# Kernel tuning notes

Measured on AMD Instinct MI355X. Metric: run time of the kernel, lower is better.

The kernel has to match this reference:

```python
import jax, jax.numpy as jnp
import numpy as np

N_SRC = 100000
N_DST = 20000
E = 1250000
D_IN = 64
D_OUT = 64
NEG_SLOPE = 0.2  # PyG GATConv default


def setup_inputs() -> dict:
    key = jax.random.key(0)
    ks = jax.random.split(key, 8)
    x = jax.random.normal(ks[0], (N_SRC, D_IN), dtype=jnp.float32)
    res_n_id = jax.random.randint(ks[1], (N_DST,), 0, N_SRC)
    edge_src = jax.random.randint(ks[2], (E,), 0, N_SRC)
    edge_dst = jax.random.randint(ks[3], (E,), 0, N_DST)
    W = jax.random.normal(ks[4], (D_IN, D_OUT), dtype=jnp.float32) / np.sqrt(D_IN)
    att_src = jax.random.normal(ks[5], (D_OUT,), dtype=jnp.float32)
    att_dst = jax.random.normal(ks[6], (D_OUT,), dtype=jnp.float32)
    bias = jax.random.normal(ks[7], (D_OUT,), dtype=jnp.float32) * 0.01
    return {"x": x, "res_n_id": res_n_id, "edge_src": edge_src,
            "edge_dst": edge_dst, "W": W, "att_src": att_src,
            "att_dst": att_dst, "bias": bias}


def reference(x, res_n_id, edge_src, edge_dst, W, att_src, att_dst, bias):
    # Shared linear transform (in_channels is an int -> one weight in PyG)
    h_src = x @ W                      # [N_src, D_OUT]
    h_dst = x[res_n_id] @ W            # [N_dst, D_OUT]
    # Per-node attention logits
    a_src = h_src @ att_src            # [N_src]
    a_dst = h_dst @ att_dst            # [N_dst]
    # Per-edge attention score (gather)
    e = jax.nn.leaky_relu(a_src[edge_src] + a_dst[edge_dst], NEG_SLOPE)  # [E]
    # Segment softmax over incoming edges of each destination node
    m = jax.ops.segment_max(e, edge_dst, num_segments=N_DST)             # [N_dst]
    ex = jnp.exp(e - m[edge_dst])
    denom = jax.ops.segment_sum(ex, edge_dst, num_segments=N_DST)        # [N_dst]
    alpha = ex / (denom[edge_dst] + 1e-16)                               # [E]
    # (dropout on alpha is eval-mode identity)
    # Weighted scatter-aggregate
    msg = h_src[edge_src] * alpha[:, None]                               # [E, D_OUT]
    out = jax.ops.segment_sum(msg, edge_dst, num_segments=N_DST)         # [N_dst, D_OUT]
    return out + bias
```

## Files before the change

kernel.cpp:

```cpp
#include <hip/hip_runtime.h>

#define N_SRC 100000
#define N_DST 20000
#define NE    1250000
#define D     64
#define NEG_SLOPE 0.2f

#define NBKT 2500
#define BCAP 768
#define TILE 4096
#define GEMM_BLKS 391
#define ADST_BLKS 79

__device__ __forceinline__ unsigned short f2bf(float f) {
    unsigned u = __float_as_uint(f);
    u += 0x7FFFu + ((u >> 16) & 1);
    return (unsigned short)(u >> 16);
}
__device__ __forceinline__ float blo(unsigned u) { return __uint_as_float(u << 16); }
__device__ __forceinline__ float bhi(unsigned u) { return __uint_as_float(u & 0xFFFF0000u); }

__global__ __launch_bounds__(256) void k_pre(const float* __restrict__ W,
                                             const float* __restrict__ att_src,
                                             const float* __restrict__ att_dst,
                                             const float* __restrict__ x,
                                             const int* __restrict__ res_n_id,
                                             unsigned short* __restrict__ xb,
                                             float* __restrict__ a_src,
                                             float* __restrict__ a_dst) {
    __shared__ __align__(16) float wL[D];
    int t = threadIdx.x, blk = blockIdx.x;
    bool isA = blk < GEMM_BLKS;
    if (t < D) {
        const float* att = isA ? att_src : att_dst;
        float s = 0.f;
#pragma unroll
        for (int c = 0; c < D; ++c) s += W[t * D + c] * att[c];
        wL[t] = s;
    }
    __syncthreads();
    const float4* x4 = (const float4*)x;
    if (isA) {
        int w = t >> 6, lane = t & 63;
        int row0 = blk * 256 + w * 64;
        ushort4* xb4 = (ushort4*)xb;
        float4 wv = *((const float4*)wL + (lane & 15));
#pragma unroll 4
        for (int it = 0; it < 16; ++it) {
            int r4 = row0 + it * 4;
            if (r4 >= N_SRC) break;
            float4 v = x4[(size_t)r4 * 16 + lane];
            ushort4 o;
            o.x = f2bf(v.x); o.y = f2bf(v.y); o.z = f2bf(v.z); o.w = f2bf(v.w);
            xb4[(size_t)r4 * 16 + lane] = o;
            float p = v.x * wv.x + v.y * wv.y + v.z * wv.z + v.w * wv.w;
            p += __shfl_xor(p, 1, 64); p += __shfl_xor(p, 2, 64);
            p += __shfl_xor(p, 4, 64); p += __shfl_xor(p, 8, 64);
            if ((lane & 15) == 0) a_src[r4 + (lane >> 4)] = p;
        }
    } else {
        int bi = blk - GEMM_BLKS;
        int grp = t >> 4, il = t & 15;
        float4 wv = *((const float4*)wL + il);
        for (int j = bi * 256 + grp; j < bi * 256 + 256; j += 16) {
            if (j < N_DST) {
                int row = res_n_id[j];
                float4 v = x4[(size_t)row * 16 + il];
                float p = v.x * wv.x + v.y * wv.y + v.z * wv.z + v.w * wv.w;
                p += __shfl_xor(p, 1, 64); p += __shfl_xor(p, 2, 64);
                p += __shfl_xor(p, 4, 64); p += __shfl_xor(p, 8, 64);
                if (il == 0) a_dst[j] = p;
            }
        }
    }
}

__global__ __launch_bounds__(1024) void k_bucket(const int* __restrict__ es,
                                                 const int* __restrict__ ed,
                                                 int* __restrict__ gcur,
                                                 int* __restrict__ buf) {
    __shared__ int hist[NBKT];
    __shared__ int lofs[NBKT];
    __shared__ int gbase[NBKT];
    __shared__ int wtot[16];
    __shared__ int stage[TILE];
    int t = threadIdx.x;
    int w = t >> 6, lane = t & 63;
    int base = blockIdx.x * TILE;
    int nE = NE - base; if (nE > TILE) nE = TILE;

    for (int i = t; i < NBKT; i += 1024) hist[i] = 0;
    __syncthreads();

    int s_[4], d_[4], rk_[4];
#pragma unroll
    for (int j = 0; j < 4; ++j) {
        int i = t + 1024 * j;
        d_[j] = -1;
        if (i < nE) {
            s_[j] = es[base + i];
            d_[j] = ed[base + i];
            rk_[j] = atomicAdd(&hist[d_[j] >> 3], 1);
        }
    }
    __syncthreads();

    int c0 = t * 3;
    int hc[3] = {0, 0, 0};
#pragma unroll
    for (int j = 0; j < 3; ++j)
        if (c0 + j < NBKT) hc[j] = hist[c0 + j];
    int sum = hc[0] + hc[1] + hc[2];
    int incl = sum;
#pragma unroll
    for (int off = 1; off < 64; off <<= 1) {
        int u = __shfl_up(incl, off, 64);
        if (lane >= off) incl += u;
    }
    if (lane == 63) wtot[w] = incl;
    __syncthreads();
    int wpre = 0;
#pragma unroll
    for (int j = 0; j < 16; ++j) wpre += (j < w) ? wtot[j] : 0;
    {
        int run = wpre + incl - sum;
#pragma unroll
        for (int j = 0; j < 3; ++j) {
            int b = c0 + j;
            if (b < NBKT) {
                lofs[b] = run;
                gbase[b] = hc[j] ? atomicAdd(&gcur[b], hc[j]) : 0;
                run += hc[j];
            }
        }
    }
    __syncthreads();

#pragma unroll
    for (int j = 0; j < 4; ++j) {
        if (d_[j] >= 0) {
            int b = d_[j] >> 3;
            stage[lofs[b] + rk_[j]] = s_[j] | ((d_[j] & 7) << 17) | (b << 20);
        }
    }
    __syncthreads();

    for (int idx = t; idx < nE; idx += 1024) {
        int rec = stage[idx];
        int b = ((unsigned)rec) >> 20;
        int off = gbase[b] + idx - lofs[b];
        if (off < BCAP) buf[b * BCAP + off] = rec;
    }
}

__global__ __launch_bounds__(256) void k_aggB(const int* __restrict__ buf,
                                              const int* __restrict__ gcur,
                                              const float* __restrict__ a_src,
                                              const float* __restrict__ a_dst,
                                              const unsigned short* __restrict__ xb,
                                              const float* __restrict__ W,
                                              const float* __restrict__ bias,
                                              float* __restrict__ out) {
    __shared__ int2 sorted[BCAP];
    __shared__ float Ws[D * D];
    __shared__ float yL[4][D];
    __shared__ int  scw[8 * 4];
    __shared__ int  begs[9];
    int bk = blockIdx.x;
    int t = threadIdx.x;
    int w = t >> 6, lane = t & 63;
    {
        const float4* W4 = (const float4*)W;
        float4* Ws4 = (float4*)Ws;
#pragma unroll
        for (int p = 0; p < 4; ++p) Ws4[t + 256 * p] = W4[t + 256 * p];
    }
    int n = gcur[bk];
    if (n > BCAP) n = BCAP;

    const int* src = buf + (size_t)bk * BCAP;
    int r0 = 0, r1 = 0, r2 = 0;
    int bin0 = -1, bin1 = -1, bin2 = -1;
    if (t < n)       { r0 = src[t];       bin0 = (r0 >> 17) & 7; }
    if (t + 256 < n) { r1 = src[t + 256]; bin1 = (r1 >> 17) & 7; }
    if (t + 512 < n) { r2 = src[t + 512]; bin2 = (r2 >> 17) & 7; }

    int h[8], incl[8];
#pragma unroll
    for (int i = 0; i < 8; ++i)
        h[i] = (bin0 == i) + (bin1 == i) + (bin2 == i);

#pragma unroll
    for (int i = 0; i < 8; ++i) {
        int v = h[i];
#pragma unroll
        for (int off = 1; off < 64; off <<= 1) {
            int u = __shfl_up(v, off, 64);
            if (lane >= off) v += u;
        }
        incl[i] = v;
        int tot = __shfl(v, 63, 64);
        if (lane == 0) scw[i * 4 + w] = tot;
    }
    __syncthreads();

    if (t < 32) {
        int v = scw[t];
#pragma unroll
        for (int off = 1; off < 32; off <<= 1) {
            int u = __shfl_up(v, off, 64);
            if (t >= off) v += u;
        }
        scw[t] = v;
    }
    __syncthreads();
    if (t < 8) begs[t] = (t == 0) ? 0 : scw[t * 4 - 1];
    if (t == 8) begs[8] = n;

    int p0 = 0, p1 = 0, p2 = 0;
#pragma unroll
    for (int i = 0; i < 8; ++i) {
        int idx = i * 4 + w;
        int base_i = ((idx ? scw[idx - 1] : 0)) + (incl[i] - h[i]);
        p0 += (bin0 == i) ? base_i : 0;
        p1 += (bin1 == i) ? base_i : 0;
        p2 += (bin2 == i) ? base_i : 0;
    }
    p1 += (bin1 == bin0);
    p2 += (bin2 == bin0) + (bin2 == bin1);
    if (bin0 >= 0) sorted[p0].x = r0;
    if (bin1 >= 0) sorted[p1].x = r1;
    if (bin2 >= 0) sorted[p2].x = r2;
    __syncthreads();

    int g = lane >> 3, il = lane & 7;
    float bsv = bias[lane];
#pragma unroll
    for (int q = 0; q < 2; ++q) {
        int dlo = w * 2 + q;
        int beg = begs[dlo], end = begs[dlo + 1];
        float ad = a_dst[bk * 8 + dlo];

        for (int i = beg + lane; i < end; i += 64) {
            int meta = sorted[i].x;
            float v = a_src[meta & 0x1FFFF] + ad;
            v = v > 0.f ? v : NEG_SLOPE * v;
            sorted[i].y = __float_as_int(__expf(v));
        }
        __builtin_amdgcn_wave_barrier();

        float a0 = 0.f, a1 = 0.f, a2 = 0.f, a3 = 0.f;
        float a4c = 0.f, a5 = 0.f, a6 = 0.f, a7 = 0.f;
        float den = 0.f;
        int i = beg;
        for (; i + 32 <= end; i += 32) {
            int2 ra = sorted[i + g];
            int2 rb = sorted[i + 8 + g];
            int2 rc = sorted[i + 16 + g];
            int2 rd = sorted[i + 24 + g];
            const uint4 ha = *(const uint4*)(xb + (size_t)(ra.x & 0x1FFFF) * D + 8 * il);
            const uint4 hc4 = *(const uint4*)(xb + (size_t)(rb.x & 0x1FFFF) * D + 8 * il);
            const uint4 he = *(const uint4*)(xb + (size_t)(rc.x & 0x1FFFF) * D + 8 * il);
            const uint4 hf = *(const uint4*)(xb + (size_t)(rd.x & 0x1FFFF) * D + 8 * il);
            float ea = __int_as_float(ra.y);
            float eb = __int_as_float(rb.y);
            float ec = __int_as_float(rc.y);
            float ed = __int_as_float(rd.y);
            a0 = fmaf(ea, blo(ha.x), a0); a1 = fmaf(ea, bhi(ha.x), a1);
            a2 = fmaf(ea, blo(ha.y), a2); a3 = fmaf(ea, bhi(ha.y), a3);
            a4c = fmaf(ea, blo(ha.z), a4c); a5 = fmaf(ea, bhi(ha.z), a5);
            a6 = fmaf(ea, blo(ha.w), a6); a7 = fmaf(ea, bhi(ha.w), a7);
            a0 = fmaf(eb, blo(hc4.x), a0); a1 = fmaf(eb, bhi(hc4.x), a1);
            a2 = fmaf(eb, blo(hc4.y), a2); a3 = fmaf(eb, bhi(hc4.y), a3);
            a4c = fmaf(eb, blo(hc4.z), a4c); a5 = fmaf(eb, bhi(hc4.z), a5);
            a6 = fmaf(eb, blo(hc4.w), a6); a7 = fmaf(eb, bhi(hc4.w), a7);
            a0 = fmaf(ec, blo(he.x), a0); a1 = fmaf(ec, bhi(he.x), a1);
            a2 = fmaf(ec, blo(he.y), a2); a3 = fmaf(ec, bhi(he.y), a3);
            a4c = fmaf(ec, blo(he.z), a4c); a5 = fmaf(ec, bhi(he.z), a5);
            a6 = fmaf(ec, blo(he.w), a6); a7 = fmaf(ec, bhi(he.w), a7);
            a0 = fmaf(ed, blo(hf.x), a0); a1 = fmaf(ed, bhi(hf.x), a1);
            a2 = fmaf(ed, blo(hf.y), a2); a3 = fmaf(ed, bhi(hf.y), a3);
            a4c = fmaf(ed, blo(hf.z), a4c); a5 = fmaf(ed, bhi(hf.z), a5);
            a6 = fmaf(ed, blo(hf.w), a6); a7 = fmaf(ed, bhi(hf.w), a7);
            den += (ea + eb) + (ec + ed);
        }
        for (; i + 16 <= end; i += 16) {
            int2 ra = sorted[i + g];
            int2 rb = sorted[i + 8 + g];
            const uint4 ha = *(const uint4*)(xb + (size_t)(ra.x & 0x1FFFF) * D + 8 * il);
            const uint4 hc4 = *(const uint4*)(xb + (size_t)(rb.x & 0x1FFFF) * D + 8 * il);
            float ea = __int_as_float(ra.y);
            float eb = __int_as_float(rb.y);
            a0 = fmaf(ea, blo(ha.x), a0); a1 = fmaf(ea, bhi(ha.x), a1);
            a2 = fmaf(ea, blo(ha.y), a2); a3 = fmaf(ea, bhi(ha.y), a3);
            a4c = fmaf(ea, blo(ha.z), a4c); a5 = fmaf(ea, bhi(ha.z), a5);
            a6 = fmaf(ea, blo(ha.w), a6); a7 = fmaf(ea, bhi(ha.w), a7);
            a0 = fmaf(eb, blo(hc4.x), a0); a1 = fmaf(eb, bhi(hc4.x), a1);
            a2 = fmaf(eb, blo(hc4.y), a2); a3 = fmaf(eb, bhi(hc4.y), a3);
            a4c = fmaf(eb, blo(hc4.z), a4c); a5 = fmaf(eb, bhi(hc4.z), a5);
            a6 = fmaf(eb, blo(hc4.w), a6); a7 = fmaf(eb, bhi(hc4.w), a7);
            den += ea + eb;
        }
        for (; i < end; i += 8) {
            int idx = i + g;
            bool ok = idx < end;
            float e = 0.f;
            if (ok) {
                int2 r = sorted[idx];
                e = __int_as_float(r.y);
                const uint4 hv = *(const uint4*)(xb + (size_t)(r.x & 0x1FFFF) * D + 8 * il);
                a0 = fmaf(e, blo(hv.x), a0); a1 = fmaf(e, bhi(hv.x), a1);
                a2 = fmaf(e, blo(hv.y), a2); a3 = fmaf(e, bhi(hv.y), a3);
                a4c = fmaf(e, blo(hv.z), a4c); a5 = fmaf(e, bhi(hv.z), a5);
                a6 = fmaf(e, blo(hv.w), a6); a7 = fmaf(e, bhi(hv.w), a7);
            }
            den += e;
        }
#pragma unroll
        for (int off = 8; off <= 32; off <<= 1) {
            a0 += __shfl_xor(a0, off, 64); a1 += __shfl_xor(a1, off, 64);
            a2 += __shfl_xor(a2, off, 64); a3 += __shfl_xor(a3, off, 64);
            a4c += __shfl_xor(a4c, off, 64); a5 += __shfl_xor(a5, off, 64);
            a6 += __shfl_xor(a6, off, 64); a7 += __shfl_xor(a7, off, 64);
            den += __shfl_xor(den, off, 64);
        }
        if (g == 0) {
            float inv = 1.f / (den + 1e-16f);
            yL[w][8 * il + 0] = a0 * inv;  yL[w][8 * il + 1] = a1 * inv;
            yL[w][8 * il + 2] = a2 * inv;  yL[w][8 * il + 3] = a3 * inv;
            yL[w][8 * il + 4] = a4c * inv; yL[w][8 * il + 5] = a5 * inv;
            yL[w][8 * il + 6] = a6 * inv;  yL[w][8 * il + 7] = a7 * inv;
        }
        __builtin_amdgcn_wave_barrier();
        float o = 0.f;
#pragma unroll 8
        for (int k = 0; k < D; ++k)
            o = fmaf(yL[w][k], Ws[k * D + lane], o);
        out[((size_t)bk * 8 + dlo) * D + lane] = o + bsv;
        __builtin_amdgcn_wave_barrier();
    }
}

extern "C" void kernel_launch(void* const* d_in, const int* in_sizes, int n_in,
                              void* d_out, int out_size, void* d_ws, size_t ws_size,
                              hipStream_t stream) {
    const float* x        = (const float*)d_in[0];
    const int*   res_n_id = (const int*)d_in[1];
    const int*   edge_src = (const int*)d_in[2];
    const int*   edge_dst = (const int*)d_in[3];
    const float* W        = (const float*)d_in[4];
    const float* att_src  = (const float*)d_in[5];
    const float* att_dst  = (const float*)d_in[6];
    const float* bias     = (const float*)d_in[7];
    float* out = (float*)d_out;

    char* w = (char*)d_ws;
    unsigned short* xb = (unsigned short*)w; w += (size_t)N_SRC * D * 2;
    int*   buf   = (int*)w;   w += (size_t)NBKT * BCAP * 4;
    float* a_src = (float*)w; w += (size_t)N_SRC * 4;
    float* a_dst = (float*)w; w += (size_t)N_DST * 4;
    int*   gcur  = (int*)w;   w += (size_t)NBKT * 4;

    hipMemsetAsync(gcur, 0, NBKT * sizeof(int), stream);
    k_pre<<<GEMM_BLKS + ADST_BLKS, 256, 0, stream>>>(W, att_src, att_dst, x,
                                                     res_n_id, xb, a_src, a_dst);
    k_bucket<<<(NE + TILE - 1) / TILE, 1024, 0, stream>>>(edge_src, edge_dst, gcur, buf);
    k_aggB<<<NBKT, 256, 0, stream>>>(buf, gcur, a_src, a_dst, xb, W, bias, out);
}
```

Before: 160.8 us.

## Fuse preprocessing and edge bucketing into one heterogeneous kernel launch

Merges the projection/bf16-conversion kernel and the edge-bucketing kernel into a single launch, with disjoint block ranges doing bucketing, a_src/xb conversion, and a_dst computation concurrently. The bucketing tile doubles to 8192 edges per block (153 blocks), and the GEMM/adst blocks are enlarged to 1024 threads. This removes one kernel launch and the serialization between two independent stages, so the two can overlap on the GPU. In exchange, shared memory per block is larger (the union is sized by the bucketing layout), and fewer, larger bucketing blocks may lower occupancy and add more register pressure from the 8-element per-thread arrays.

```diff
diff --git a/kernel.cpp b/kernel.cpp
--- a/kernel.cpp
+++ b/kernel.cpp
@@ -8,9 +8,10 @@
 
 #define NBKT 2500
 #define BCAP 768
-#define TILE 4096
-#define GEMM_BLKS 391
-#define ADST_BLKS 79
+#define TILE 8192
+#define BUCKET_BLKS 153
+#define GEMM_BLKS 98
+#define ADST_BLKS 20
 
 __device__ __forceinline__ unsigned short f2bf(float f) {
     unsigned u = __float_as_uint(f);
@@ -20,31 +21,112 @@
 __device__ __forceinline__ float blo(unsigned u) { return __uint_as_float(u << 16); }
 __device__ __forceinline__ float bhi(unsigned u) { return __uint_as_float(u & 0xFFFF0000u); }
 
-__global__ __launch_bounds__(256) void k_pre(const float* __restrict__ W,
-                                             const float* __restrict__ att_src,
-                                             const float* __restrict__ att_dst,
-                                             const float* __restrict__ x,
-                                             const int* __restrict__ res_n_id,
-                                             unsigned short* __restrict__ xb,
-                                             float* __restrict__ a_src,
-                                             float* __restrict__ a_dst) {
-    __shared__ __align__(16) float wL[D];
-    int t = threadIdx.x, blk = blockIdx.x;
-    bool isA = blk < GEMM_BLKS;
-    if (t < D) {
-        const float* att = isA ? att_src : att_dst;
-        float s = 0.f;
-#pragma unroll
-        for (int c = 0; c < D; ++c) s += W[t * D + c] * att[c];
-        wL[t] = s;
-    }
-    __syncthreads();
-    const float4* x4 = (const float4*)x;
-    if (isA) {
-        int w = t >> 6, lane = t & 63;
-        int row0 = blk * 256 + w * 64;
+__global__ __launch_bounds__(1024) void k_fused(const int* __restrict__ es,
+                                                const int* __restrict__ ed,
+                                                int* __restrict__ gcur,
+                                                int* __restrict__ buf,
+                                                const float* __restrict__ W,
+                                                const float* __restrict__ att_src,
+                                                const float* __restrict__ att_dst,
+                                                const float* __restrict__ x,
+                                                const int* __restrict__ res_n_id,
+                                                unsigned short* __restrict__ xb,
+                                                float* __restrict__ a_src,
+                                                float* __restrict__ a_dst) {
+    __shared__ union U {
+        struct {
+            int hist[NBKT];
+            int lofs[NBKT];
+            int gbase[NBKT];
+            int wtot[16];
+            int stage[TILE];
+        } b;
+        __align__(16) float wL[D];
+    } sm;
+    int t = threadIdx.x;
+    int blk = blockIdx.x;
+    int w = t >> 6, lane = t & 63;
+
+    if (blk < BUCKET_BLKS) {
+        int base = blk * TILE;
+        int nE = NE - base; if (nE > TILE) nE = TILE;
+
+        for (int i = t; i < NBKT; i += 1024) sm.b.hist[i] = 0;
+        __syncthreads();
+
+        int s_[8], d_[8], rk_[8];
+#pragma unroll
+        for (int j = 0; j < 8; ++j) {
+            int i = t + 1024 * j;
+            d_[j] = -1;
+            if (i < nE) {
+                s_[j] = es[base + i];
+                d_[j] = ed[base + i];
+                rk_[j] = atomicAdd(&sm.b.hist[d_[j] >> 3], 1);
+            }
+        }
+        __syncthreads();
+
+        int c0 = t * 3;
+        int hc[3] = {0, 0, 0};
+#pragma unroll
+        for (int j = 0; j < 3; ++j)
+            if (c0 + j < NBKT) hc[j] = sm.b.hist[c0 + j];
+        int sum = hc[0] + hc[1] + hc[2];
+        int incl = sum;
+#pragma unroll
+        for (int off = 1; off < 64; off <<= 1) {
+            int u = __shfl_up(incl, off, 64);
+            if (lane >= off) incl += u;
+        }
+        if (lane == 63) sm.b.wtot[w] = incl;
+        __syncthreads();
+        int wpre = 0;
+#pragma unroll
+        for (int j = 0; j < 16; ++j) wpre += (j < w) ? sm.b.wtot[j] : 0;
+        {
+            int run = wpre + incl - sum;
+#pragma unroll
+            for (int j = 0; j < 3; ++j) {
+                int b = c0 + j;
+                if (b < NBKT) {
+                    sm.b.lofs[b] = run;
+                    sm.b.gbase[b] = hc[j] ? atomicAdd(&gcur[b], hc[j]) : 0;
+                    run += hc[j];
+                }
+            }
+        }
+        __syncthreads();
+
+#pragma unroll
+        for (int j = 0; j < 8; ++j) {
+            if (d_[j] >= 0) {
+                int b = d_[j] >> 3;
+                sm.b.stage[sm.b.lofs[b] + rk_[j]] =
+                    s_[j] | ((d_[j] & 7) << 17) | (b << 20);
+            }
+        }
+        __syncthreads();
+
+        for (int idx = t; idx < nE; idx += 1024) {
+            int rec = sm.b.stage[idx];
+            int b = ((unsigned)rec) >> 20;
+            int off = sm.b.gbase[b] + idx - sm.b.lofs[b];
+            if (off < BCAP) buf[b * BCAP + off] = rec;
+        }
+    } else if (blk < BUCKET_BLKS + GEMM_BLKS) {
+        int gb = blk - BUCKET_BLKS;
+        if (t < D) {
+            float s = 0.f;
+#pragma unroll
+            for (int c = 0; c < D; ++c) s += W[t * D + c] * att_src[c];
+            sm.wL[t] = s;
+        }
+        __syncthreads();
+        const float4* x4 = (const float4*)x;
         ushort4* xb4 = (ushort4*)xb;
-        float4 wv = *((const float4*)wL + (lane & 15));
+        int row0 = (gb * 16 + w) * 64;
+        float4 wv = *((const float4*)sm.wL + (lane & 15));
 #pragma unroll 4
         for (int it = 0; it < 16; ++it) {
             int r4 = row0 + it * 4;
@@ -59,97 +141,25 @@
             if ((lane & 15) == 0) a_src[r4 + (lane >> 4)] = p;
         }
     } else {
-        int bi = blk - GEMM_BLKS;
+        int ab = blk - BUCKET_BLKS - GEMM_BLKS;
+        if (t < D) {
+            float s = 0.f;
+#pragma unroll
+            for (int c = 0; c < D; ++c) s += W[t * D + c] * att_dst[c];
+            sm.wL[t] = s;
+        }
+        __syncthreads();
+        const float4* x4 = (const float4*)x;
         int grp = t >> 4, il = t & 15;
-        float4 wv = *((const float4*)wL + il);
-        for (int j = bi * 256 + grp; j < bi * 256 + 256; j += 16) {
-            if (j < N_DST) {
-                int row = res_n_id[j];
-                float4 v = x4[(size_t)row * 16 + il];
-                float p = v.x * wv.x + v.y * wv.y + v.z * wv.z + v.w * wv.w;
-                p += __shfl_xor(p, 1, 64); p += __shfl_xor(p, 2, 64);
-                p += __shfl_xor(p, 4, 64); p += __shfl_xor(p, 8, 64);
-                if (il == 0) a_dst[j] = p;
-            }
-        }
-    }
-}
-
-__global__ __launch_bounds__(1024) void k_bucket(const int* __restrict__ es,
-                                                 const int* __restrict__ ed,
-                                                 int* __restrict__ gcur,
-                                                 int* __restrict__ buf) {
-    __shared__ int hist[NBKT];
-    __shared__ int lofs[NBKT];
-    __shared__ int gbase[NBKT];
-    __shared__ int wtot[16];
-    __shared__ int stage[TILE];
-    int t = threadIdx.x;
-    int w = t >> 6, lane = t & 63;
-    int base = blockIdx.x * TILE;
-    int nE = NE - base; if (nE > TILE) nE = TILE;
-
-    for (int i = t; i < NBKT; i += 1024) hist[i] = 0;
-    __syncthreads();
-
-    int s_[4], d_[4], rk_[4];
-#pragma unroll
-    for (int j = 0; j < 4; ++j) {
-        int i = t + 1024 * j;
-        d_[j] = -1;
-        if (i < nE) {
-            s_[j] = es[base + i];
-            d_[j] = ed[base + i];
-            rk_[j] = atomicAdd(&hist[d_[j] >> 3], 1);
-        }
-    }
-    __syncthreads();
-
-    int c0 = t * 3;
-    int hc[3] = {0, 0, 0};
-#pragma unroll
-    for (int j = 0; j < 3; ++j)
-        if (c0 + j < NBKT) hc[j] = hist[c0 + j];
-    int sum = hc[0] + hc[1] + hc[2];
-    int incl = sum;
-#pragma unroll
-    for (int off = 1; off < 64; off <<= 1) {
-        int u = __shfl_up(incl, off, 64);
-        if (lane >= off) incl += u;
-    }
-    if (lane == 63) wtot[w] = incl;
-    __syncthreads();
-    int wpre = 0;
-#pragma unroll
-    for (int j = 0; j < 16; ++j) wpre += (j < w) ? wtot[j] : 0;
-    {
-        int run = wpre + incl - sum;
-#pragma unroll
-        for (int j = 0; j < 3; ++j) {
-            int b = c0 + j;
-            if (b < NBKT) {
-                lofs[b] = run;
-                gbase[b] = hc[j] ? atomicAdd(&gcur[b], hc[j]) : 0;
-                run += hc[j];
-            }
-        }
-    }
-    __syncthreads();
-
-#pragma unroll
-    for (int j = 0; j < 4; ++j) {
-        if (d_[j] >= 0) {
-            int b = d_[j] >> 3;
-            stage[lofs[b] + rk_[j]] = s_[j] | ((d_[j] & 7) << 17) | (b << 20);
-        }
-    }
-    __syncthreads();
-
-    for (int idx = t; idx < nE; idx += 1024) {
-        int rec = stage[idx];
-        int b = ((unsigned)rec) >> 20;
-        int off = gbase[b] + idx - lofs[b];
-        if (off < BCAP) buf[b * BCAP + off] = rec;
+        float4 wv = *((const float4*)sm.wL + il);
+        for (int j = ab * 64 + grp; j < N_DST; j += ADST_BLKS * 64) {
+            int row = res_n_id[j];
+            float4 v = x4[(size_t)row * 16 + il];
+            float p = v.x * wv.x + v.y * wv.y + v.z * wv.z + v.w * wv.w;
+            p += __shfl_xor(p, 1, 64); p += __shfl_xor(p, 2, 64);
+            p += __shfl_xor(p, 4, 64); p += __shfl_xor(p, 8, 64);
+            if (il == 0) a_dst[j] = p;
+        }
     }
 }
 
@@ -362,8 +372,8 @@
     int*   gcur  = (int*)w;   w += (size_t)NBKT * 4;
 
     hipMemsetAsync(gcur, 0, NBKT * sizeof(int), stream);
-    k_pre<<<GEMM_BLKS + ADST_BLKS, 256, 0, stream>>>(W, att_src, att_dst, x,
-                                                     res_n_id, xb, a_src, a_dst);
-    k_bucket<<<(NE + TILE - 1) / TILE, 1024, 0, stream>>>(edge_src, edge_dst, gcur, buf);
+    k_fused<<<BUCKET_BLKS + GEMM_BLKS + ADST_BLKS, 1024, 0, stream>>>(
+        edge_src, edge_dst, gcur, buf, W, att_src, att_dst, x, res_n_id,
+        xb, a_src, a_dst);
     k_aggB<<<NBKT, 256, 0, stream>>>(buf, gcur, a_src, a_dst, xb, W, bias, out);
 }
```

Result: faster. 146.9 us (-8.6%).
